# Kernel optimization log

Measured on AMD Instinct MI355X. Metric: run time of the kernel, lower is better.

The kernel has to match this reference:

```python
import jax, jax.numpy as jnp
import numpy as np

B, T_ENC, D, T_MEL, NMEL, R = 256, 200, 256, 1000, 80, 5
IN_R = NMEL * R  # 400


def _gru(x, h, Wih, bih, Whh, bhh):
    gi = x @ Wih.T + bih
    gh = h @ Whh.T + bhh
    ir, iz, inn = jnp.split(gi, 3, axis=-1)
    hr, hz, hn = jnp.split(gh, 3, axis=-1)
    r = jax.nn.sigmoid(ir + hr)
    z = jax.nn.sigmoid(iz + hz)
    n = jnp.tanh(inn + r * hn)
    return (1.0 - z) * n + z * h


def setup_inputs() -> dict:
    key = jax.random.key(0)
    ks = jax.random.split(key, 32)
    s = 0.05
    d = {
        'encoder_outputs': jax.random.normal(ks[0], (B, T_ENC, D), jnp.float32),
        'inputs': jax.random.normal(ks[1], (B, T_MEL, NMEL), jnp.float32),
        'memory_lengths': jax.random.randint(ks[2], (B,), 100, T_ENC + 1),
        # prenet
        'prenet_W1': jax.random.normal(ks[3], (256, IN_R)) * s,
        'prenet_b1': jnp.zeros((256,)),
        'prenet_W2': jax.random.normal(ks[4], (128, 256)) * s,
        'prenet_b2': jnp.zeros((128,)),
        # attention GRUCell (input 128+256=384)
        'attn_Wih': jax.random.normal(ks[5], (768, 384)) * s,
        'attn_bih': jnp.zeros((768,)),
        'attn_Whh': jax.random.normal(ks[6], (768, 256)) * s,
        'attn_bhh': jnp.zeros((768,)),
        # memory layer + Bahdanau attention
        'mem_W': jax.random.normal(ks[7], (256, 256)) * s,
        'query_W': jax.random.normal(ks[8], (256, 256)) * s,
        'v_W': jax.random.normal(ks[9], (256,)) * s,
        # project_to_decoder_in
        'proj_in_W': jax.random.normal(ks[10], (256, 512)) * s,
        'proj_in_b': jnp.zeros((256,)),
        # 2 decoder GRUCells
        'dec1_Wih': jax.random.normal(ks[11], (768, 256)) * s,
        'dec1_bih': jnp.zeros((768,)),
        'dec1_Whh': jax.random.normal(ks[12], (768, 256)) * s,
        'dec1_bhh': jnp.zeros((768,)),
        'dec2_Wih': jax.random.normal(ks[13], (768, 256)) * s,
        'dec2_bih': jnp.zeros((768,)),
        'dec2_Whh': jax.random.normal(ks[14], (768, 256)) * s,
        'dec2_bhh': jnp.zeros((768,)),
        # proj_to_mel
        'mel_W': jax.random.normal(ks[15], (IN_R, 256)) * s,
        'mel_b': jnp.zeros((IN_R,)),
    }
    return d


def reference(encoder_outputs, inputs, memory_lengths,
              prenet_W1, prenet_b1, prenet_W2, prenet_b2,
              attn_Wih, attn_bih, attn_Whh, attn_bhh,
              mem_W, query_W, v_W, proj_in_W, proj_in_b,
              dec1_Wih, dec1_bih, dec1_Whh, dec1_bhh,
              dec2_Wih, dec2_bih, dec2_Whh, dec2_bhh,
              mel_W, mel_b):
    Bn, Tenc, _ = encoder_outputs.shape
    Tm = inputs.shape[1]
    T = Tm - Tm % R
    inputs_r = inputs[:, :T, :].reshape(Bn, T // R, IN_R)  # [B, Td, 400]
    Td = T // R

    processed_memory = encoder_outputs @ mem_W.T  # [B, Tenc, 256]
    mask = jnp.arange(Tenc)[None, :] >= memory_lengths[:, None]  # True => masked

    # teacher forcing: input at step 0 is zeros, then shifted targets
    prev = jnp.concatenate(
        [jnp.zeros((Bn, 1, IN_R), inputs.dtype), inputs_r[:, :-1, :]], axis=1)
    prev = prev.transpose(1, 0, 2)  # [Td, B, 400]

    def step(carry, cur_in):
        attn_h, h1, h2, attention = carry
        # prenet (dropout = identity at eval)
        x = jax.nn.relu(cur_in @ prenet_W1.T + prenet_b1)
        x = jax.nn.relu(x @ prenet_W2.T + prenet_b2)  # [B,128]
        cell_in = jnp.concatenate([x, attention], axis=-1)  # [B,384]
        attn_h = _gru(cell_in, attn_h, attn_Wih, attn_bih, attn_Whh, attn_bhh)
        # Bahdanau additive attention
        q = attn_h @ query_W.T  # [B,256]
        score = jnp.tanh(processed_memory + q[:, None, :]) @ v_W  # [B,Tenc]
        score = jnp.where(mask, -1e9, score)
        align = jax.nn.softmax(score, axis=-1)
        attention = jnp.einsum('bt,btd->bd', align, encoder_outputs)
        d = jnp.concatenate([attn_h, attention], axis=-1) @ proj_in_W.T + proj_in_b
        h1 = _gru(d, h1, dec1_Wih, dec1_bih, dec1_Whh, dec1_bhh)
        d = h1 + d
        h2 = _gru(d, h2, dec2_Wih, dec2_bih, dec2_Whh, dec2_bhh)
        d = h2 + d
        out = d @ mel_W.T + mel_b  # [B,400]
        return (attn_h, h1, h2, attention), (out, align)

    z = jnp.zeros((Bn, 256), encoder_outputs.dtype)
    init = (z, z, z, z)
    _, (outs, aligns) = jax.lax.scan(step, init, prev)
    outputs = outs.transpose(1, 0, 2)      # [B, Td, 400]
    alignments = aligns.transpose(1, 0, 2)  # [B, Td, Tenc]
    return outputs, alignments
```

## Files before the change

kernel.cpp:

```cpp
#include <hip/hip_runtime.h>
#include <math.h>

#define ALIGN_OFF 20480000

typedef __fp16 h2_t __attribute__((ext_vector_type(2)));

__device__ __forceinline__ float sigf(float x) {
    return __builtin_amdgcn_rcpf(1.0f + __expf(-x));
}
__device__ __forceinline__ float tanhff(float x) {
    float e = __expf(2.0f * x);
    return 1.0f - 2.0f * __builtin_amdgcn_rcpf(e + 1.0f);
}
__device__ __forceinline__ unsigned short f2bf(float x) {
    unsigned u = __float_as_uint(x);
    return (unsigned short)((u + 0x7FFFu + ((u >> 16) & 1u)) >> 16);
}
__device__ __forceinline__ float blo(unsigned u) { return __uint_as_float(u << 16); }
__device__ __forceinline__ float bhi(unsigned u) { return __uint_as_float(u & 0xffff0000u); }
__device__ __forceinline__ unsigned pkh(float a, float b) {
    h2_t r = __builtin_amdgcn_cvt_pkrtz(a, b);
    return __builtin_bit_cast(unsigned, r);
}
__device__ __forceinline__ float dot2(unsigned w, unsigned a, float c) {
#if __has_builtin(__builtin_amdgcn_fdot2)
    return __builtin_amdgcn_fdot2(__builtin_bit_cast(h2_t, w),
                                  __builtin_bit_cast(h2_t, a), c, false);
#else
    h2_t wv = __builtin_bit_cast(h2_t, w), av = __builtin_bit_cast(h2_t, a);
    return c + (float)wv.x * (float)av.x + (float)wv.y * (float)av.y;
#endif
}

template<int AMODE, int EPI>
__global__ __launch_bounds__(256)
void gemm128(const float* __restrict__ A, int lda,
             const float* __restrict__ W, int ldw,
             const float* __restrict__ bias,
             float* __restrict__ C, int ldc, int M, int N, int K)
{
    __shared__ float As[16][128];
    __shared__ float Bs[16][128];
    const int m0 = blockIdx.x * 128, n0 = blockIdx.y * 128;
    const int tid = threadIdx.x;
    const int tx = tid & 15, ty = tid >> 4;
    float acc[8][8] = {};
    for (int k0 = 0; k0 < K; k0 += 16) {
        {
            const int m = tid >> 1, h = (tid & 1) * 8;
            const int grow = m0 + m;
            float4 a0, a1;
            if (AMODE == 2) {
                int t = grow >> 8, b = grow & 255;
                if (t == 0) { a0 = make_float4(0, 0, 0, 0); a1 = a0; }
                else {
                    const float* p = A + (size_t)b * 80000 + (t - 1) * 400 + k0 + h;
                    a0 = *(const float4*)p; a1 = *(const float4*)(p + 4);
                }
            } else {
                const float* p = A + (size_t)grow * lda + k0 + h;
                a0 = *(const float4*)p; a1 = *(const float4*)(p + 4);
            }
            As[h + 0][m] = a0.x; As[h + 1][m] = a0.y; As[h + 2][m] = a0.z; As[h + 3][m] = a0.w;
            As[h + 4][m] = a1.x; As[h + 5][m] = a1.y; As[h + 6][m] = a1.z; As[h + 7][m] = a1.w;
            const int gn = n0 + m;
            float4 b0, b1;
            if (gn < N) {
                const float* p = W + (size_t)gn * ldw + k0 + h;
                b0 = *(const float4*)p; b1 = *(const float4*)(p + 4);
            } else { b0 = make_float4(0, 0, 0, 0); b1 = b0; }
            Bs[h + 0][m] = b0.x; Bs[h + 1][m] = b0.y; Bs[h + 2][m] = b0.z; Bs[h + 3][m] = b0.w;
            Bs[h + 4][m] = b1.x; Bs[h + 5][m] = b1.y; Bs[h + 6][m] = b1.z; Bs[h + 7][m] = b1.w;
        }
        __syncthreads();
        #pragma unroll
        for (int kk = 0; kk < 16; ++kk) {
            float av[8], bv[8];
            *(float4*)&av[0] = *(const float4*)&As[kk][ty * 8];
            *(float4*)&av[4] = *(const float4*)&As[kk][ty * 8 + 4];
            *(float4*)&bv[0] = *(const float4*)&Bs[kk][tx * 8];
            *(float4*)&bv[4] = *(const float4*)&Bs[kk][tx * 8 + 4];
            #pragma unroll
            for (int i = 0; i < 8; ++i)
                #pragma unroll
                for (int j = 0; j < 8; ++j)
                    acc[i][j] += av[i] * bv[j];
        }
        __syncthreads();
    }
    #pragma unroll
    for (int i = 0; i < 8; ++i) {
        const int row = m0 + ty * 8 + i;
        const int t_ = row >> 8, b_ = row & 255;
        #pragma unroll
        for (int j4 = 0; j4 < 2; ++j4) {
            const int col = n0 + tx * 8 + j4 * 4;
            if (col >= N) continue;
            float4 v;
            float* pv = &v.x;
            #pragma unroll
            for (int u = 0; u < 4; ++u) {
                float x = acc[i][j4 * 4 + u] + (bias ? bias[col + u] : 0.0f);
                if (EPI == 1 || EPI == 4) x = fmaxf(x, 0.0f);
                pv[u] = x;
            }
            if (EPI == 2)      *(float4*)(C + (size_t)b_ * 80000 + t_ * 400 + col) = v;
            else if (EPI == 3) {
                ushort4 o;
                o.x = f2bf(pv[0]); o.y = f2bf(pv[1]); o.z = f2bf(pv[2]); o.w = f2bf(pv[3]);
                *(ushort4*)((unsigned short*)C + (size_t)row * 256 + col) = o;
            } else if (EPI == 4) {
                uint2 o; o.x = pkh(pv[0], pv[1]); o.y = pkh(pv[2], pv[3]);
                *(uint2*)((unsigned*)C + (size_t)row * 64 + (col >> 1)) = o;
            } else *(float4*)(C + (size_t)row * ldc + col) = v;
        }
    }
}

__global__ __launch_bounds__(256)
void pack_wh(const float* __restrict__ W, uint4* __restrict__ P, int N, int K)
{
    const int tot = N * (K >> 3);
    for (int i = blockIdx.x * 256 + threadIdx.x; i < tot; i += gridDim.x * 256) {
        const int n = i % N, k8 = i / N;
        const float* s = W + (size_t)n * K + (k8 << 3);
        uint4 o;
        o.x = pkh(s[0], s[1]); o.y = pkh(s[2], s[3]);
        o.z = pkh(s[4], s[5]); o.w = pkh(s[6], s[7]);
        P[(size_t)k8 * N + n] = o;
    }
}

__global__ __launch_bounds__(256)
void pack_bf16(const float* __restrict__ src, unsigned short* __restrict__ dst, int n)
{
    for (int i = (blockIdx.x * 256 + threadIdx.x) * 4; i < n; i += gridDim.x * 1024) {
        float4 v = *(const float4*)(src + i);
        ushort4 o;
        o.x = f2bf(v.x); o.y = f2bf(v.y); o.z = f2bf(v.z); o.w = f2bf(v.w);
        *(ushort4*)(dst + i) = o;
    }
}

__global__ __launch_bounds__(768)
void decoder_loop(
    const uint4* __restrict__ X2h4,
    const unsigned short* __restrict__ pmH,
    const unsigned short* __restrict__ encH,
    const int*   __restrict__ mlen,
    const uint4* __restrict__ aWihH, const float* __restrict__ abih,
    const uint4* __restrict__ aWhhH, const float* __restrict__ abhh,
    const uint4* __restrict__ qWH,   const float* __restrict__ vW,
    const uint4* __restrict__ pjWH,  const float* __restrict__ pjb,
    const uint4* __restrict__ w1ihH, const float* __restrict__ w1bih,
    const uint4* __restrict__ w1hhH, const float* __restrict__ w1bhh,
    const uint4* __restrict__ w2ihH, const float* __restrict__ w2bih,
    const uint4* __restrict__ w2hhH, const float* __restrict__ w2bhh,
    float* __restrict__ dall, float* __restrict__ alout)
{
    __shared__ unsigned short pmS[51200];
    __shared__ uint4 xcat[48];
    __shared__ unsigned ha_h[128], h1_h[128], h2_h[128], d0_h[128], d1_h[128];
    __shared__ float hA[256], h1s[256], h2s[256], d0s[256], d1s[256];
    __shared__ float qv[256], vvS[256];
    __shared__ float sc[200], al[208];
    __shared__ float gi[768], gh[768];
    __shared__ float part[12][256];

    const int b = blockIdx.x, tid = threadIdx.x;
    const int wv = tid >> 6, ln = tid & 63;
    const unsigned short* encG = encH + (size_t)b * 51200;

    {
        const uint4* psrc = (const uint4*)(pmH + (size_t)b * 51200);
        for (int i = tid; i < 6400; i += 768) ((uint4*)pmS)[i] = psrc[i];
        if (tid < 256) { vvS[tid] = vW[tid]; hA[tid] = 0.f; h1s[tid] = 0.f; h2s[tid] = 0.f; }
        if (tid < 128) { ha_h[tid] = 0u; h1_h[tid] = 0u; h2_h[tid] = 0u; }
        if (tid < 32)  xcat[16 + tid] = make_uint4(0, 0, 0, 0);
    }
    const int len = mlen[b];
    __syncthreads();

    for (int t = 0; t < 200; ++t) {
        if (tid < 16) xcat[tid] = X2h4[((size_t)t * 256 + b) * 16 + tid];
        __syncthreads();
        {
            float ai = 0.f, ah = 0.f;
            const uint4* wp = aWihH + tid;
            #pragma unroll 8
            for (int k8 = 0; k8 < 48; ++k8) {
                const uint4 w = wp[(size_t)k8 * 768], a = xcat[k8];
                ai = dot2(w.x, a.x, ai); ai = dot2(w.y, a.y, ai);
                ai = dot2(w.z, a.z, ai); ai = dot2(w.w, a.w, ai);
            }
            const uint4* wq = aWhhH + tid;
            const uint4* hc = (const uint4*)ha_h;
            #pragma unroll 8
            for (int k8 = 0; k8 < 32; ++k8) {
                const uint4 w = wq[(size_t)k8 * 768], a = hc[k8];
                ah = dot2(w.x, a.x, ah); ah = dot2(w.y, a.y, ah);
                ah = dot2(w.z, a.z, ah); ah = dot2(w.w, a.w, ah);
            }
            gi[tid] = ai + abih[tid];
            gh[tid] = ah + abhh[tid];
        }
        __syncthreads();
        if (tid < 256) {
            const float r = sigf(gi[tid] + gh[tid]);
            const float z = sigf(gi[256 + tid] + gh[256 + tid]);
            const float n = tanhff(gi[512 + tid] + r * gh[512 + tid]);
            const float hp = (1.f - z) * n + z * hA[tid];
            hA[tid] = hp;
            const float hq = __shfl_down(hp, 1);
            if (!(tid & 1)) ha_h[tid >> 1] = pkh(hp, hq);
        }
        __syncthreads();

        if (tid < 256) {
            float s = 0.f;
            const uint4* qp = qWH + tid;
            const uint4* hc = (const uint4*)ha_h;
            #pragma unroll 8
            for (int k8 = 0; k8 < 32; ++k8) {
                const uint4 w = qp[(size_t)k8 * 256], a = hc[k8];
                s = dot2(w.x, a.x, s); s = dot2(w.y, a.y, s);
                s = dot2(w.z, a.z, s); s = dot2(w.w, a.w, s);
            }
            qv[tid] = s;
        }
        __syncthreads();
        {
            const float4 q4 = ((const float4*)qv)[ln];
            const float4 v4 = ((const float4*)vvS)[ln];
            for (int i = wv; i < 200; i += 12) {
                if (i < len) {
                    const uint2 pr = *(const uint2*)(pmS + i * 256 + ln * 4);
                    float p = v4.x * tanhff(blo(pr.x) + q4.x)
                            + v4.y * tanhff(bhi(pr.x) + q4.y)
                            + v4.z * tanhff(blo(pr.y) + q4.z)
                            + v4.w * tanhff(bhi(pr.y) + q4.w);
                    #pragma unroll
                    for (int off = 32; off; off >>= 1) p += __shfl_down(p, off);
                    if (ln == 0) sc[i] = p;
                } else if (ln == 0) sc[i] = -1e9f;
            }
        }
        __syncthreads();
        if (wv == 0) {
            float v0 = sc[ln], v1 = sc[ln + 64], v2 = sc[ln + 128];
            float v3 = (ln < 8) ? sc[ln + 192] : -1e30f;
            float mx = fmaxf(fmaxf(v0, v1), fmaxf(v2, v3));
            #pragma unroll
            for (int off = 32; off; off >>= 1) mx = fmaxf(mx, __shfl_xor(mx, off));
            float e0 = __expf(v0 - mx), e1 = __expf(v1 - mx), e2 = __expf(v2 - mx);
            float e3 = (ln < 8) ? __expf(v3 - mx) : 0.f;
            float ss = e0 + e1 + e2 + e3;
            #pragma unroll
            for (int off = 32; off; off >>= 1) ss += __shfl_xor(ss, off);
            const float inv = 1.0f / ss;
            float* ao = alout + (size_t)b * 40000 + (size_t)t * 200;
            al[ln]       = e0 * inv; ao[ln]       = e0 * inv;
            al[ln + 64]  = e1 * inv; ao[ln + 64]  = e1 * inv;
            al[ln + 128] = e2 * inv; ao[ln + 128] = e2 * inv;
            if (ln < 8) { al[ln + 192] = e3 * inv; ao[ln + 192] = e3 * inv; }
        }
        __syncthreads();
        {
            float a0 = 0.f, a1 = 0.f, a2 = 0.f, a3 = 0.f;
            for (int i = wv; i < len; i += 12) {
                const float w = al[i];
                const uint2 ev = *(const uint2*)(encG + i * 256 + ln * 4);
                a0 = fmaf(w, blo(ev.x), a0); a1 = fmaf(w, bhi(ev.x), a1);
                a2 = fmaf(w, blo(ev.y), a2); a3 = fmaf(w, bhi(ev.y), a3);
            }
            ((float4*)part)[wv * 64 + ln] = make_float4(a0, a1, a2, a3);
        }
        __syncthreads();
        if (tid < 256) {
            float s = 0.f;
            #pragma unroll
            for (int w2 = 0; w2 < 12; ++w2) s += part[w2][tid];
            const float s1 = __shfl_down(s, 1);
            if (!(tid & 1)) ((unsigned*)xcat)[64 + (tid >> 1)] = pkh(s, s1);
        }
        __syncthreads();

        if (tid < 512) {
            const int half = tid >> 8, idx = tid & 255;
            const uint4* wp = pjWH + (size_t)half * 32 * 256 + idx;
            const uint4* src = half ? (const uint4*)(xcat + 16) : (const uint4*)ha_h;
            float s = 0.f;
            #pragma unroll 8
            for (int k8 = 0; k8 < 32; ++k8) {
                const uint4 w = wp[(size_t)k8 * 256], a = src[k8];
                s = dot2(w.x, a.x, s); s = dot2(w.y, a.y, s);
                s = dot2(w.z, a.z, s); s = dot2(w.w, a.w, s);
            }
            part[half][idx] = s;
        }
        __syncthreads();
        if (tid < 256) {
            const float d0 = part[0][tid] + part[1][tid] + pjb[tid];
            d0s[tid] = d0;
            const float dq = __shfl_down(d0, 1);
            if (!(tid & 1)) d0_h[tid >> 1] = pkh(d0, dq);
        }
        __syncthreads();

        {
            float ai = 0.f, ah = 0.f;
            const uint4* wp = w1ihH + tid;
            const uint4* xc = (const uint4*)d0_h;
            #pragma unroll 8
            for (int k8 = 0; k8 < 32; ++k8) {
                const uint4 w = wp[(size_t)k8 * 768], a = xc[k8];
                ai = dot2(w.x, a.x, ai); ai = dot2(w.y, a.y, ai);
                ai = dot2(w.z, a.z, ai); ai = dot2(w.w, a.w, ai);
            }
            const uint4* wq = w1hhH + tid;
            const uint4* hc = (const uint4*)h1_h;
            #pragma unroll 8
            for (int k8 = 0; k8 < 32; ++k8) {
                const uint4 w = wq[(size_t)k8 * 768], a = hc[k8];
                ah = dot2(w.x, a.x, ah); ah = dot2(w.y, a.y, ah);
                ah = dot2(w.z, a.z, ah); ah = dot2(w.w, a.w, ah);
            }
            gi[tid] = ai + w1bih[tid];
            gh[tid] = ah + w1bhh[tid];
        }
        __syncthreads();
        if (tid < 256) {
            const float r = sigf(gi[tid] + gh[tid]);
            const float z = sigf(gi[256 + tid] + gh[256 + tid]);
            const float n = tanhff(gi[512 + tid] + r * gh[512 + tid]);
            const float hp = (1.f - z) * n + z * h1s[tid];
            h1s[tid] = hp;
            const float d1 = hp + d0s[tid];
            d1s[tid] = d1;
            const float hq = __shfl_down(hp, 1);
            const float dq = __shfl_down(d1, 1);
            if (!(tid & 1)) { h1_h[tid >> 1] = pkh(hp, hq); d1_h[tid >> 1] = pkh(d1, dq); }
        }
        __syncthreads();

        {
            float ai = 0.f, ah = 0.f;
            const uint4* wp = w2ihH + tid;
            const uint4* xc = (const uint4*)d1_h;
            #pragma unroll 8
            for (int k8 = 0; k8 < 32; ++k8) {
                const uint4 w = wp[(size_t)k8 * 768], a = xc[k8];
                ai = dot2(w.x, a.x, ai); ai = dot2(w.y, a.y, ai);
                ai = dot2(w.z, a.z, ai); ai = dot2(w.w, a.w, ai);
            }
            const uint4* wq = w2hhH + tid;
            const uint4* hc = (const uint4*)h2_h;
            #pragma unroll 8
            for (int k8 = 0; k8 < 32; ++k8) {
                const uint4 w = wq[(size_t)k8 * 768], a = hc[k8];
                ah = dot2(w.x, a.x, ah); ah = dot2(w.y, a.y, ah);
                ah = dot2(w.z, a.z, ah); ah = dot2(w.w, a.w, ah);
            }
            gi[tid] = ai + w2bih[tid];
            gh[tid] = ah + w2bhh[tid];
        }
        __syncthreads();
        if (tid < 256) {
            const float r = sigf(gi[tid] + gh[tid]);
            const float z = sigf(gi[256 + tid] + gh[256 + tid]);
            const float n = tanhff(gi[512 + tid] + r * gh[512 + tid]);
            const float hp = (1.f - z) * n + z * h2s[tid];
            h2s[tid] = hp;
            dall[((size_t)t * 256 + b) * 256 + tid] = hp + d1s[tid];
            const float hq = __shfl_down(hp, 1);
            if (!(tid & 1)) h2_h[tid >> 1] = pkh(hp, hq);
        }
        __syncthreads();
    }
}

extern "C" void kernel_launch(void* const* d_in, const int* in_sizes, int n_in,
                              void* d_out, int out_size, void* d_ws, size_t ws_size,
                              hipStream_t stream)
{
    const float* enc    = (const float*)d_in[0];
    const float* inputs = (const float*)d_in[1];
    const int*   mlen   = (const int*)d_in[2];
    const float* pW1 = (const float*)d_in[3];  const float* pb1 = (const float*)d_in[4];
    const float* pW2 = (const float*)d_in[5];  const float* pb2 = (const float*)d_in[6];
    const float* aWih = (const float*)d_in[7]; const float* abih = (const float*)d_in[8];
    const float* aWhh = (const float*)d_in[9]; const float* abhh = (const float*)d_in[10];
    const float* memW = (const float*)d_in[11];
    const float* qW   = (const float*)d_in[12];
    const float* vW   = (const float*)d_in[13];
    const float* pjW  = (const float*)d_in[14]; const float* pjb = (const float*)d_in[15];
    const float* w1ih = (const float*)d_in[16]; const float* w1bih = (const float*)d_in[17];
    const float* w1hh = (const float*)d_in[18]; const float* w1bhh = (const float*)d_in[19];
    const float* w2ih = (const float*)d_in[20]; const float* w2bih = (const float*)d_in[21];
    const float* w2hh = (const float*)d_in[22]; const float* w2bhh = (const float*)d_in[23];
    const float* melW = (const float*)d_in[24]; const float* melb = (const float*)d_in[25];

    float* out = (float*)d_out;
    float* ws  = (float*)d_ws;

    float* X1   = ws;
    float* dall = X1;
    unsigned* X2h = (unsigned*)(ws + 13107200);
    unsigned short* pmH  = (unsigned short*)(ws + 16384000);
    unsigned short* encH = (unsigned short*)(ws + 22937600);
    uint4* aWihH = (uint4*)(ws + 29491200);
    uint4* aWhhH = aWihH + 36864;
    uint4* w1ihH = aWhhH + 24576;
    uint4* w1hhH = w1ihH + 24576;
    uint4* w2ihH = w1hhH + 24576;
    uint4* w2hhH = w2ihH + 24576;
    uint4* pjWH  = w2hhH + 24576;
    uint4* qWH   = pjWH + 16384;

    pack_wh<<<64, 256, 0, stream>>>(aWih, aWihH, 768, 384);
    pack_wh<<<64, 256, 0, stream>>>(aWhh, aWhhH, 768, 256);
    pack_wh<<<64, 256, 0, stream>>>(w1ih, w1ihH, 768, 256);
    pack_wh<<<64, 256, 0, stream>>>(w1hh, w1hhH, 768, 256);
    pack_wh<<<64, 256, 0, stream>>>(w2ih, w2ihH, 768, 256);
    pack_wh<<<64, 256, 0, stream>>>(w2hh, w2hhH, 768, 256);
    pack_wh<<<64, 256, 0, stream>>>(pjW,  pjWH,  256, 512);
    pack_wh<<<64, 256, 0, stream>>>(qW,   qWH,   256, 256);
    pack_bf16<<<1024, 256, 0, stream>>>(enc, encH, 13107200);

    gemm128<2, 1><<<dim3(400, 2), 256, 0, stream>>>(
        inputs, 0, pW1, 400, pb1, X1, 256, 51200, 256, 400);
    gemm128<0, 4><<<dim3(400, 1), 256, 0, stream>>>(
        X1, 256, pW2, 256, pb2, (float*)X2h, 128, 51200, 128, 256);
    gemm128<0, 3><<<dim3(400, 2), 256, 0, stream>>>(
        enc, 256, memW, 256, nullptr, (float*)pmH, 256, 51200, 256, 256);

    decoder_loop<<<256, 768, 0, stream>>>(
        (const uint4*)X2h, pmH, encH, mlen,
        aWihH, abih, aWhhH, abhh, qWH, vW, pjWH, pjb,
        w1ihH, w1bih, w1hhH, w1bhh, w2ihH, w2bih, w2hhH, w2bhh,
        dall, out + ALIGN_OFF);

    gemm128<0, 2><<<dim3(400, 4), 256, 0, stream>>>(
        dall, 256, melW, 256, melb, out, 400, 51200, 400, 256);
}
```

Before: 7.994 ms.

## Split GRU matvecs across 8-block groups with global flag barriers

Each group of 8 blocks now shares 8 batch rows. Each block computes a 1/8 slice of the gate outputs for all 8 rows, so weight reads are reused across rows instead of every block streaming the full weight matrices. Hidden states and activations are exchanged through a global double-buffered plane, using cache-bypassing loads and stores plus spin-wait flag barriers. This adds four inter-block barriers per timestep and relies on all 256 blocks being co-resident, which risks deadlock or barrier latency dominating.

```diff
diff --git a/kernel.cpp b/kernel.cpp
--- a/kernel.cpp
+++ b/kernel.cpp
@@ -2,6 +2,7 @@
 #include <math.h>
 
 #define ALIGN_OFF 20480000
+#define FLS 32
 
 typedef __fp16 h2_t __attribute__((ext_vector_type(2)));
 
@@ -30,6 +31,20 @@
     h2_t wv = __builtin_bit_cast(h2_t, w), av = __builtin_bit_cast(h2_t, a);
     return c + (float)wv.x * (float)av.x + (float)wv.y * (float)av.y;
 #endif
+}
+__device__ __forceinline__ float dot8(uint4 w, uint4 a, float c) {
+    c = dot2(w.x, a.x, c); c = dot2(w.y, a.y, c);
+    c = dot2(w.z, a.z, c); return dot2(w.w, a.w, c);
+}
+
+__device__ __forceinline__ uint4 ld_dev_u4(const unsigned* p) {
+    uint4 r;
+    asm volatile("global_load_dwordx4 %0, %1, off sc0 sc1\n\ts_waitcnt vmcnt(0)"
+                 : "=&v"(r) : "v"(p) : "memory");
+    return r;
+}
+__device__ __forceinline__ void st_dev_u1(unsigned* p, unsigned v) {
+    asm volatile("global_store_dword %0, %1, off sc0 sc1" :: "v"(p), "v"(v) : "memory");
 }
 
 template<int AMODE, int EPI>
@@ -132,6 +147,22 @@
 }
 
 __global__ __launch_bounds__(256)
+void pack_whp(const float* __restrict__ W, uint4* __restrict__ P, int K)
+{
+    const int tot = 768 * (K >> 3);
+    for (int i = blockIdx.x * 256 + threadIdx.x; i < tot; i += gridDim.x * 256) {
+        const int n = i % 768, k8 = i / 768;
+        const int c = n & 255, kind = n >> 8;
+        const int p = (c >> 5) * 96 + kind * 32 + (c & 31);
+        const float* s = W + (size_t)n * K + (k8 << 3);
+        uint4 o;
+        o.x = pkh(s[0], s[1]); o.y = pkh(s[2], s[3]);
+        o.z = pkh(s[4], s[5]); o.w = pkh(s[6], s[7]);
+        P[(size_t)k8 * 768 + p] = o;
+    }
+}
+
+__global__ __launch_bounds__(256)
 void pack_bf16(const float* __restrict__ src, unsigned short* __restrict__ dst, int n)
 {
     for (int i = (blockIdx.x * 256 + threadIdx.x) * 4; i < n; i += gridDim.x * 1024) {
@@ -140,6 +171,23 @@
         o.x = f2bf(v.x); o.y = f2bf(v.y); o.z = f2bf(v.z); o.w = f2bf(v.w);
         *(ushort4*)(dst + i) = o;
     }
+}
+
+__device__ __forceinline__ void gbar(unsigned* flags, int g, int j,
+                                     unsigned target, int tid)
+{
+    __syncthreads();
+    if (tid == 0) {
+        asm volatile("s_waitcnt vmcnt(0)" ::: "memory");
+        __hip_atomic_store(flags + (size_t)(g * 8 + j) * FLS, target,
+                           __ATOMIC_RELAXED, __HIP_MEMORY_SCOPE_AGENT);
+    }
+    if (tid < 8) {
+        const unsigned* f = flags + (size_t)(g * 8 + tid) * FLS;
+        while (__hip_atomic_load(f, __ATOMIC_RELAXED, __HIP_MEMORY_SCOPE_AGENT) < target)
+            __builtin_amdgcn_s_sleep(1);
+    }
+    __syncthreads();
 }
 
 __global__ __launch_bounds__(768)
@@ -148,84 +196,109 @@
     const unsigned short* __restrict__ pmH,
     const unsigned short* __restrict__ encH,
     const int*   __restrict__ mlen,
-    const uint4* __restrict__ aWihH, const float* __restrict__ abih,
-    const uint4* __restrict__ aWhhH, const float* __restrict__ abhh,
-    const uint4* __restrict__ qWH,   const float* __restrict__ vW,
-    const uint4* __restrict__ pjWH,  const float* __restrict__ pjb,
-    const uint4* __restrict__ w1ihH, const float* __restrict__ w1bih,
-    const uint4* __restrict__ w1hhH, const float* __restrict__ w1bhh,
-    const uint4* __restrict__ w2ihH, const float* __restrict__ w2bih,
-    const uint4* __restrict__ w2hhH, const float* __restrict__ w2bhh,
+    const uint4* __restrict__ aWihP, const float* __restrict__ abih,
+    const uint4* __restrict__ aWhhP, const float* __restrict__ abhh,
+    const uint4* __restrict__ qWP,   const float* __restrict__ vW,
+    const uint4* __restrict__ pjWP,  const float* __restrict__ pjb,
+    const uint4* __restrict__ w1ihP, const float* __restrict__ w1bih,
+    const uint4* __restrict__ w1hhP, const float* __restrict__ w1bhh,
+    const uint4* __restrict__ w2ihP, const float* __restrict__ w2bih,
+    const uint4* __restrict__ w2hhP, const float* __restrict__ w2bhh,
+    unsigned* __restrict__ plane,
+    unsigned* __restrict__ flags,
     float* __restrict__ dall, float* __restrict__ alout)
 {
     __shared__ unsigned short pmS[51200];
-    __shared__ uint4 xcat[48];
-    __shared__ unsigned ha_h[128], h1_h[128], h2_h[128], d0_h[128], d1_h[128];
-    __shared__ float hA[256], h1s[256], h2s[256], d0s[256], d1s[256];
-    __shared__ float qv[256], vvS[256];
-    __shared__ float sc[200], al[208];
-    __shared__ float gi[768], gh[768];
-    __shared__ float part[12][256];
-
-    const int b = blockIdx.x, tid = threadIdx.x;
+    __shared__ uint4 act4[8][80];
+    __shared__ uint4 hrow4[32];
+    __shared__ float scratch[3072];
+    __shared__ float locA[256], loc1[256], loc2[256], locD0[256], locD1[256];
+    __shared__ float qv[256], vvS[256], sc[200], al[208];
+
+    const int bid = blockIdx.x, tid = threadIdx.x;
+    const int g = bid >> 3, j = bid & 7;
+    const int row0 = g * 8;
+    const int myrow = row0 + j;
     const int wv = tid >> 6, ln = tid & 63;
-    const unsigned short* encG = encH + (size_t)b * 51200;
+    const int ri = tid / 96;
+    const int cj = tid - ri * 96;
+    const int kind = cj >> 5, off = cj & 31;
+    const int gidx = kind * 256 + j * 32 + off;
+    const int pcol = j * 96 + cj;
+    const unsigned short* encG = encH + (size_t)myrow * 51200;
+
+    unsigned* hA_buf = plane;
+    unsigned* h1_buf = plane + 65536;
+    unsigned* h2_buf = plane + 131072;
+    unsigned* attP   = plane + 196608;
+    unsigned* d0P    = plane + 229376;
+    unsigned* d1P    = plane + 262144;
 
     {
-        const uint4* psrc = (const uint4*)(pmH + (size_t)b * 51200);
-        for (int i = tid; i < 6400; i += 768) ((uint4*)pmS)[i] = psrc[i];
-        if (tid < 256) { vvS[tid] = vW[tid]; hA[tid] = 0.f; h1s[tid] = 0.f; h2s[tid] = 0.f; }
-        if (tid < 128) { ha_h[tid] = 0u; h1_h[tid] = 0u; h2_h[tid] = 0u; }
-        if (tid < 32)  xcat[16 + tid] = make_uint4(0, 0, 0, 0);
-    }
-    const int len = mlen[b];
+        const uint4* ps = (const uint4*)(pmH + (size_t)myrow * 51200);
+        for (int i = tid; i < 6400; i += 768) ((uint4*)pmS)[i] = ps[i];
+        if (tid < 256) {
+            vvS[tid] = vW[tid];
+            locA[tid] = 0.f; loc1[tid] = 0.f; loc2[tid] = 0.f;
+            locD0[tid] = 0.f; locD1[tid] = 0.f;
+        }
+    }
+    const int len = mlen[myrow];
+    unsigned bt = 0;
     __syncthreads();
 
     for (int t = 0; t < 200; ++t) {
-        if (tid < 16) xcat[tid] = X2h4[((size_t)t * 256 + b) * 16 + tid];
+        const int cur = t & 1, prv = cur ^ 1;
+        unsigned* hA_w = hA_buf + cur * 32768;
+        const unsigned* hA_r = hA_buf + prv * 32768;
+        unsigned* h1_w = h1_buf + cur * 32768;
+        const unsigned* h1_r = h1_buf + prv * 32768;
+        unsigned* h2_w = h2_buf + cur * 32768;
+        const unsigned* h2_r = h2_buf + prv * 32768;
+
+        if (tid < 128) {
+            const int r_ = tid >> 4, c_ = tid & 15;
+            act4[r_][c_] = X2h4[((size_t)t * 256 + row0 + r_) * 16 + c_];
+        } else if (tid < 384) {
+            const int i = tid - 128, r_ = i >> 5, c_ = i & 31;
+            act4[r_][16 + c_] = ld_dev_u4(attP + (size_t)(row0 + r_) * 128 + 4 * c_);
+        } else if (tid < 640) {
+            const int i = tid - 384, r_ = i >> 5, c_ = i & 31;
+            act4[r_][48 + c_] = ld_dev_u4(hA_r + (size_t)(row0 + r_) * 128 + 4 * c_);
+        }
         __syncthreads();
         {
             float ai = 0.f, ah = 0.f;
-            const uint4* wp = aWihH + tid;
-            #pragma unroll 8
-            for (int k8 = 0; k8 < 48; ++k8) {
-                const uint4 w = wp[(size_t)k8 * 768], a = xcat[k8];
-                ai = dot2(w.x, a.x, ai); ai = dot2(w.y, a.y, ai);
-                ai = dot2(w.z, a.z, ai); ai = dot2(w.w, a.w, ai);
-            }
-            const uint4* wq = aWhhH + tid;
-            const uint4* hc = (const uint4*)ha_h;
-            #pragma unroll 8
-            for (int k8 = 0; k8 < 32; ++k8) {
-                const uint4 w = wq[(size_t)k8 * 768], a = hc[k8];
-                ah = dot2(w.x, a.x, ah); ah = dot2(w.y, a.y, ah);
-                ah = dot2(w.z, a.z, ah); ah = dot2(w.w, a.w, ah);
-            }
-            gi[tid] = ai + abih[tid];
-            gh[tid] = ah + abhh[tid];
-        }
-        __syncthreads();
-        if (tid < 256) {
-            const float r = sigf(gi[tid] + gh[tid]);
-            const float z = sigf(gi[256 + tid] + gh[256 + tid]);
-            const float n = tanhff(gi[512 + tid] + r * gh[512 + tid]);
-            const float hp = (1.f - z) * n + z * hA[tid];
-            hA[tid] = hp;
+            const uint4* wp = aWihP + pcol;
+            #pragma unroll 8
+            for (int k8 = 0; k8 < 48; ++k8) ai = dot8(wp[(size_t)k8 * 768], act4[ri][k8], ai);
+            const uint4* wq = aWhhP + pcol;
+            #pragma unroll 8
+            for (int k8 = 0; k8 < 32; ++k8) ah = dot8(wq[(size_t)k8 * 768], act4[ri][48 + k8], ah);
+            scratch[ri * 96 + cj] = ai + abih[gidx];
+            scratch[768 + ri * 96 + cj] = ah + abhh[gidx];
+        }
+        __syncthreads();
+        if (tid < 256) {
+            const int nri = tid >> 5, noff = tid & 31, base = nri * 96;
+            const float rr = sigf(scratch[base + noff] + scratch[768 + base + noff]);
+            const float zz = sigf(scratch[base + 32 + noff] + scratch[768 + base + 32 + noff]);
+            const float nn = tanhff(scratch[base + 64 + noff] + rr * scratch[768 + base + 64 + noff]);
+            const float hp = (1.f - zz) * nn + zz * locA[tid];
+            locA[tid] = hp;
             const float hq = __shfl_down(hp, 1);
-            if (!(tid & 1)) ha_h[tid >> 1] = pkh(hp, hq);
-        }
-        __syncthreads();
-
+            if (!(noff & 1))
+                st_dev_u1(hA_w + (size_t)(row0 + nri) * 128 + j * 16 + (noff >> 1), pkh(hp, hq));
+        }
+        gbar(flags, g, j, ++bt, tid);
+
+        if (tid < 32) hrow4[tid] = ld_dev_u4(hA_w + (size_t)myrow * 128 + 4 * tid);
+        __syncthreads();
         if (tid < 256) {
             float s = 0.f;
-            const uint4* qp = qWH + tid;
-            const uint4* hc = (const uint4*)ha_h;
-            #pragma unroll 8
-            for (int k8 = 0; k8 < 32; ++k8) {
-                const uint4 w = qp[(size_t)k8 * 256], a = hc[k8];
-                s = dot2(w.x, a.x, s); s = dot2(w.y, a.y, s);
-                s = dot2(w.z, a.z, s); s = dot2(w.w, a.w, s);
-            }
+            const uint4* qp = qWP + tid;
+            #pragma unroll 8
+            for (int k8 = 0; k8 < 32; ++k8) s = dot8(qp[(size_t)k8 * 256], hrow4[k8], s);
             qv[tid] = s;
         }
         __syncthreads();
@@ -240,7 +313,7 @@
                             + v4.z * tanhff(blo(pr.y) + q4.z)
                             + v4.w * tanhff(bhi(pr.y) + q4.w);
                     #pragma unroll
-                    for (int off = 32; off; off >>= 1) p += __shfl_down(p, off);
+                    for (int o = 32; o; o >>= 1) p += __shfl_down(p, o);
                     if (ln == 0) sc[i] = p;
                 } else if (ln == 0) sc[i] = -1e9f;
             }
@@ -251,14 +324,14 @@
             float v3 = (ln < 8) ? sc[ln + 192] : -1e30f;
             float mx = fmaxf(fmaxf(v0, v1), fmaxf(v2, v3));
             #pragma unroll
-            for (int off = 32; off; off >>= 1) mx = fmaxf(mx, __shfl_xor(mx, off));
+            for (int o = 32; o; o >>= 1) mx = fmaxf(mx, __shfl_xor(mx, o));
             float e0 = __expf(v0 - mx), e1 = __expf(v1 - mx), e2 = __expf(v2 - mx);
             float e3 = (ln < 8) ? __expf(v3 - mx) : 0.f;
             float ss = e0 + e1 + e2 + e3;
             #pragma unroll
-            for (int off = 32; off; off >>= 1) ss += __shfl_xor(ss, off);
+            for (int o = 32; o; o >>= 1) ss += __shfl_xor(ss, o);
             const float inv = 1.0f / ss;
-            float* ao = alout + (size_t)b * 40000 + (size_t)t * 200;
+            float* ao = alout + (size_t)myrow * 40000 + (size_t)t * 200;
             al[ln]       = e0 * inv; ao[ln]       = e0 * inv;
             al[ln + 64]  = e1 * inv; ao[ln + 64]  = e1 * inv;
             al[ln + 128] = e2 * inv; ao[ln + 128] = e2 * inv;
@@ -273,109 +346,119 @@
                 a0 = fmaf(w, blo(ev.x), a0); a1 = fmaf(w, bhi(ev.x), a1);
                 a2 = fmaf(w, blo(ev.y), a2); a3 = fmaf(w, bhi(ev.y), a3);
             }
-            ((float4*)part)[wv * 64 + ln] = make_float4(a0, a1, a2, a3);
+            ((float4*)scratch)[wv * 64 + ln] = make_float4(a0, a1, a2, a3);
         }
         __syncthreads();
         if (tid < 256) {
             float s = 0.f;
             #pragma unroll
-            for (int w2 = 0; w2 < 12; ++w2) s += part[w2][tid];
+            for (int w2 = 0; w2 < 12; ++w2) s += scratch[w2 * 256 + tid];
             const float s1 = __shfl_down(s, 1);
-            if (!(tid & 1)) ((unsigned*)xcat)[64 + (tid >> 1)] = pkh(s, s1);
-        }
-        __syncthreads();
-
+            if (!(tid & 1))
+                st_dev_u1(attP + (size_t)myrow * 128 + (tid >> 1), pkh(s, s1));
+        }
+        gbar(flags, g, j, ++bt, tid);
+
+        if (tid < 512) {
+            const int r_ = tid >> 6, c_ = tid & 63;
+            const unsigned* src = (c_ < 32)
+                ? (hA_w + (size_t)(row0 + r_) * 128 + 4 * c_)
+                : (attP + (size_t)(row0 + r_) * 128 + 4 * (c_ - 32));
+            act4[r_][c_] = ld_dev_u4(src);
+        }
+        __syncthreads();
         if (tid < 512) {
             const int half = tid >> 8, idx = tid & 255;
-            const uint4* wp = pjWH + (size_t)half * 32 * 256 + idx;
-            const uint4* src = half ? (const uint4*)(xcat + 16) : (const uint4*)ha_h;
+            const int nri = idx >> 5, noff = idx & 31;
+            const uint4* wp = pjWP + (j * 32 + noff);
             float s = 0.f;
             #pragma unroll 8
-            for (int k8 = 0; k8 < 32; ++k8) {
-                const uint4 w = wp[(size_t)k8 * 256], a = src[k8];
-                s = dot2(w.x, a.x, s); s = dot2(w.y, a.y, s);
-                s = dot2(w.z, a.z, s); s = dot2(w.w, a.w, s);
-            }
-            part[half][idx] = s;
-        }
-        __syncthreads();
-        if (tid < 256) {
-            const float d0 = part[0][tid] + part[1][tid] + pjb[tid];
-            d0s[tid] = d0;
+            for (int k8 = half * 32; k8 < half * 32 + 32; ++k8)
+                s = dot8(wp[(size_t)k8 * 256], act4[nri][k8], s);
+            scratch[half * 256 + idx] = s;
+        }
+        __syncthreads();
+        if (tid < 256) {
+            const int nri = tid >> 5, noff = tid & 31;
+            const float d0 = scratch[tid] + scratch[256 + tid] + pjb[j * 32 + noff];
+            locD0[tid] = d0;
             const float dq = __shfl_down(d0, 1);
-            if (!(tid & 1)) d0_h[tid >> 1] = pkh(d0, dq);
-        }
-        __syncthreads();
-
+            if (!(noff & 1))
+                st_dev_u1(d0P + (size_t)(row0 + nri) * 128 + j * 16 + (noff >> 1), pkh(d0, dq));
+        }
+        gbar(flags, g, j, ++bt, tid);
+
+        if (tid < 512) {
+            const int r_ = tid >> 6, c_ = tid & 63;
+            const unsigned* src = (c_ < 32)
+                ? (d0P + (size_t)(row0 + r_) * 128 + 4 * c_)
+                : (h1_r + (size_t)(row0 + r_) * 128 + 4 * (c_ - 32));
+            act4[r_][c_] = ld_dev_u4(src);
+        }
+        __syncthreads();
         {
             float ai = 0.f, ah = 0.f;
-            const uint4* wp = w1ihH + tid;
-            const uint4* xc = (const uint4*)d0_h;
-            #pragma unroll 8
-            for (int k8 = 0; k8 < 32; ++k8) {
-                const uint4 w = wp[(size_t)k8 * 768], a = xc[k8];
-                ai = dot2(w.x, a.x, ai); ai = dot2(w.y, a.y, ai);
-                ai = dot2(w.z, a.z, ai); ai = dot2(w.w, a.w, ai);
-            }
-            const uint4* wq = w1hhH + tid;
-            const uint4* hc = (const uint4*)h1_h;
-            #pragma unroll 8
-            for (int k8 = 0; k8 < 32; ++k8) {
-                const uint4 w = wq[(size_t)k8 * 768], a = hc[k8];
-                ah = dot2(w.x, a.x, ah); ah = dot2(w.y, a.y, ah);
-                ah = dot2(w.z, a.z, ah); ah = dot2(w.w, a.w, ah);
-            }
-            gi[tid] = ai + w1bih[tid];
-            gh[tid] = ah + w1bhh[tid];
-        }
-        __syncthreads();
-        if (tid < 256) {
-            const float r = sigf(gi[tid] + gh[tid]);
-            const float z = sigf(gi[256 + tid] + gh[256 + tid]);
-            const float n = tanhff(gi[512 + tid] + r * gh[512 + tid]);
-            const float hp = (1.f - z) * n + z * h1s[tid];
-            h1s[tid] = hp;
-            const float d1 = hp + d0s[tid];
-            d1s[tid] = d1;
+            const uint4* wp = w1ihP + pcol;
+            #pragma unroll 8
+            for (int k8 = 0; k8 < 32; ++k8) ai = dot8(wp[(size_t)k8 * 768], act4[ri][k8], ai);
+            const uint4* wq = w1hhP + pcol;
+            #pragma unroll 8
+            for (int k8 = 0; k8 < 32; ++k8) ah = dot8(wq[(size_t)k8 * 768], act4[ri][32 + k8], ah);
+            scratch[ri * 96 + cj] = ai + w1bih[gidx];
+            scratch[768 + ri * 96 + cj] = ah + w1bhh[gidx];
+        }
+        __syncthreads();
+        if (tid < 256) {
+            const int nri = tid >> 5, noff = tid & 31, base = nri * 96;
+            const float rr = sigf(scratch[base + noff] + scratch[768 + base + noff]);
+            const float zz = sigf(scratch[base + 32 + noff] + scratch[768 + base + 32 + noff]);
+            const float nn = tanhff(scratch[base + 64 + noff] + rr * scratch[768 + base + 64 + noff]);
+            const float hp = (1.f - zz) * nn + zz * loc1[tid];
+            loc1[tid] = hp;
+            const float d1 = hp + locD0[tid];
+            locD1[tid] = d1;
             const float hq = __shfl_down(hp, 1);
             const float dq = __shfl_down(d1, 1);
-            if (!(tid & 1)) { h1_h[tid >> 1] = pkh(hp, hq); d1_h[tid >> 1] = pkh(d1, dq); }
-        }
-        __syncthreads();
-
+            if (!(noff & 1)) {
+                st_dev_u1(h1_w + (size_t)(row0 + nri) * 128 + j * 16 + (noff >> 1), pkh(hp, hq));
+                st_dev_u1(d1P + (size_t)(row0 + nri) * 128 + j * 16 + (noff >> 1), pkh(d1, dq));
+            }
+        }
+        gbar(flags, g, j, ++bt, tid);
+
+        if (tid < 512) {
+            const int r_ = tid >> 6, c_ = tid & 63;
+            const unsigned* src = (c_ < 32)
+                ? (d1P + (size_t)(row0 + r_) * 128 + 4 * c_)
+                : (h2_r + (size_t)(row0 + r_) * 128 + 4 * (c_ - 32));
+            act4[r_][c_] = ld_dev_u4(src);
+        }
+        __syncthreads();
         {
             float ai = 0.f, ah = 0.f;
-            const uint4* wp = w2ihH + tid;
-            const uint4* xc = (const uint4*)d1_h;
-            #pragma unroll 8
-            for (int k8 = 0; k8 < 32; ++k8) {
-                const uint4 w = wp[(size_t)k8 * 768], a = xc[k8];
-                ai = dot2(w.x, a.x, ai); ai = dot2(w.y, a.y, ai);
-                ai = dot2(w.z, a.z, ai); ai = dot2(w.w, a.w, ai);
-            }
-            const uint4* wq = w2hhH + tid;
-            const uint4* hc = (const uint4*)h2_h;
-            #pragma unroll 8
-            for (int k8 = 0; k8 < 32; ++k8) {
-                const uint4 w = wq[(size_t)k8 * 768], a = hc[k8];
-                ah = dot2(w.x, a.x, ah); ah = dot2(w.y, a.y, ah);
-                ah = dot2(w.z, a.z, ah); ah = dot2(w.w, a.w, ah);
-            }
-            gi[tid] = ai + w2bih[tid];
-            gh[tid] = ah + w2bhh[tid];
-        }
-        __syncthreads();
-        if (tid < 256) {
-            const float r = sigf(gi[tid] + gh[tid]);
-            const float z = sigf(gi[256 + tid] + gh[256 + tid]);
-            const float n = tanhff(gi[512 + tid] + r * gh[512 + tid]);
-            const float hp = (1.f - z) * n + z * h2s[tid];
-            h2s[tid] = hp;
-            dall[((size_t)t * 256 + b) * 256 + tid] = hp + d1s[tid];
+            const uint4* wp = w2ihP + pcol;
+            #pragma unroll 8
+            for (int k8 = 0; k8 < 32; ++k8) ai = dot8(wp[(size_t)k8 * 768], act4[ri][k8], ai);
+            const uint4* wq = w2hhP + pcol;
+            #pragma unroll 8
+            for (int k8 = 0; k8 < 32; ++k8) ah = dot8(wq[(size_t)k8 * 768], act4[ri][32 + k8], ah);
+            scratch[ri * 96 + cj] = ai + w2bih[gidx];
+            scratch[768 + ri * 96 + cj] = ah + w2bhh[gidx];
+        }
+        __syncthreads();
+        if (tid < 256) {
+            const int nri = tid >> 5, noff = tid & 31, base = nri * 96;
+            const float rr = sigf(scratch[base + noff] + scratch[768 + base + noff]);
+            const float zz = sigf(scratch[base + 32 + noff] + scratch[768 + base + 32 + noff]);
+            const float nn = tanhff(scratch[base + 64 + noff] + rr * scratch[768 + base + 64 + noff]);
+            const float hp = (1.f - zz) * nn + zz * loc2[tid];
+            loc2[tid] = hp;
+            const float d2 = hp + locD1[tid];
+            dall[((size_t)t * 256 + row0 + nri) * 256 + j * 32 + noff] = d2;
             const float hq = __shfl_down(hp, 1);
-            if (!(tid & 1)) h2_h[tid >> 1] = pkh(hp, hq);
-        }
-        __syncthreads();
+            if (!(noff & 1))
+                st_dev_u1(h2_w + (size_t)(row0 + nri) * 128 + j * 16 + (noff >> 1), pkh(hp, hq));
+        }
     }
 }
 
@@ -408,23 +491,27 @@
     unsigned* X2h = (unsigned*)(ws + 13107200);
     unsigned short* pmH  = (unsigned short*)(ws + 16384000);
     unsigned short* encH = (unsigned short*)(ws + 22937600);
-    uint4* aWihH = (uint4*)(ws + 29491200);
-    uint4* aWhhH = aWihH + 36864;
-    uint4* w1ihH = aWhhH + 24576;
-    uint4* w1hhH = w1ihH + 24576;
-    uint4* w2ihH = w1hhH + 24576;
-    uint4* w2hhH = w2ihH + 24576;
-    uint4* pjWH  = w2hhH + 24576;
-    uint4* qWH   = pjWH + 16384;
-
-    pack_wh<<<64, 256, 0, stream>>>(aWih, aWihH, 768, 384);
-    pack_wh<<<64, 256, 0, stream>>>(aWhh, aWhhH, 768, 256);
-    pack_wh<<<64, 256, 0, stream>>>(w1ih, w1ihH, 768, 256);
-    pack_wh<<<64, 256, 0, stream>>>(w1hh, w1hhH, 768, 256);
-    pack_wh<<<64, 256, 0, stream>>>(w2ih, w2ihH, 768, 256);
-    pack_wh<<<64, 256, 0, stream>>>(w2hh, w2hhH, 768, 256);
-    pack_wh<<<64, 256, 0, stream>>>(pjW,  pjWH,  256, 512);
-    pack_wh<<<64, 256, 0, stream>>>(qW,   qWH,   256, 256);
+    uint4* aWihP = (uint4*)(ws + 29491200);
+    uint4* aWhhP = aWihP + 36864;
+    uint4* w1ihP = aWhhP + 24576;
+    uint4* w1hhP = w1ihP + 24576;
+    uint4* w2ihP = w1hhP + 24576;
+    uint4* w2hhP = w2ihP + 24576;
+    uint4* pjWP  = w2hhP + 24576;
+    uint4* qWP   = pjWP + 16384;
+    unsigned* plane = (unsigned*)(ws + 30228480);
+    unsigned* flags = (unsigned*)(ws + 30228480 + 294912);
+
+    hipMemsetAsync(plane, 0, (294912 + 8192) * sizeof(unsigned), stream);
+
+    pack_whp<<<64, 256, 0, stream>>>(aWih, aWihP, 384);
+    pack_whp<<<64, 256, 0, stream>>>(aWhh, aWhhP, 256);
+    pack_whp<<<64, 256, 0, stream>>>(w1ih, w1ihP, 256);
+    pack_whp<<<64, 256, 0, stream>>>(w1hh, w1hhP, 256);
+    pack_whp<<<64, 256, 0, stream>>>(w2ih, w2ihP, 256);
+    pack_whp<<<64, 256, 0, stream>>>(w2hh, w2hhP, 256);
+    pack_wh<<<64, 256, 0, stream>>>(pjW, pjWP, 256, 512);
+    pack_wh<<<64, 256, 0, stream>>>(qW,  qWP,  256, 256);
     pack_bf16<<<1024, 256, 0, stream>>>(enc, encH, 13107200);
 
     gemm128<2, 1><<<dim3(400, 2), 256, 0, stream>>>(
@@ -436,9 +523,9 @@
 
     decoder_loop<<<256, 768, 0, stream>>>(
         (const uint4*)X2h, pmH, encH, mlen,
-        aWihH, abih, aWhhH, abhh, qWH, vW, pjWH, pjb,
-        w1ihH, w1bih, w1hhH, w1bhh, w2ihH, w2bih, w2hhH, w2bhh,
-        dall, out + ALIGN_OFF);
+        aWihP, abih, aWhhP, abhh, qWP, vW, pjWP, pjb,
+        w1ihP, w1bih, w1hhP, w1bhh, w2ihP, w2bih, w2hhP, w2bhh,
+        plane, flags, dall, out + ALIGN_OFF);
 
     gemm128<0, 2><<<dim3(400, 4), 256, 0, stream>>>(
         dall, 256, melW, 256, melb, out, 400, 51200, 400, 256);
```

Result: slower. 14.55 ms (+82.0%).
